# Kernel tuning notes

Measured on AMD Instinct MI355X. Metric: run time of the kernel, lower is better.

## Reference

```python
import jax, jax.numpy as jnp
import numpy as np

INPUT_SIZE = 512
HIDDEN_SIZE = 1024
UPDATE_BIAS = 1.0


def setup_inputs() -> dict:
    key = jax.random.key(0)
    k1, k2, k3, k4, k5 = jax.random.split(key, 5)
    B, T, I, H = 64, 512, INPUT_SIZE, HIDDEN_SIZE
    xh = I + H
    s = 1.0 / np.sqrt(xh)  # nn.Linear default init scale
    inp = {
        "input": jax.random.normal(k1, (B, T, I), dtype=jnp.float32),
        "h0": jnp.zeros((B, H), dtype=jnp.float32),
        "W_rz": jax.random.uniform(k2, (2 * H, xh), minval=-s, maxval=s, dtype=jnp.float32),
        "b_rz": jax.random.uniform(k3, (2 * H,), minval=-s, maxval=s, dtype=jnp.float32),
        "W_h": jax.random.uniform(k4, (H, xh), minval=-s, maxval=s, dtype=jnp.float32),
        "b_h": jax.random.uniform(k5, (H,), minval=-s, maxval=s, dtype=jnp.float32),
    }
    return inp


def _gru_scan(input, h0, W_rz, b_rz, W_h, b_h):
    H = h0.shape[-1]

    def step(h, x_t):
        # x_t: [B, I], h: [B, H]
        xh = jnp.concatenate([x_t, h], axis=1)          # [B, I+H]
        rz = xh @ W_rz.T + b_rz                          # [B, 2H]
        r = jax.nn.sigmoid(rz[:, :H])
        z = jax.nn.sigmoid(rz[:, H:] + UPDATE_BIAS)
        xrh = jnp.concatenate([x_t, r * h], axis=1)      # [B, I+H]
        hhat = jnp.tanh(xrh @ W_h.T + b_h)               # [B, H]
        h_new = z * h + (1.0 - z) * hhat
        return h_new, h_new

    xs = jnp.swapaxes(input, 0, 1)                       # [T, B, I]
    _, ys = jax.lax.scan(step, h0, xs)                   # ys: [T, B, H]
    return jnp.swapaxes(ys, 0, 1)                        # [B, T, H]


def reference(input, h0, W_rz, b_rz, W_h, b_h):
    return _gru_scan(input, h0, W_rz, b_rz, W_h, b_h)
```

## Files before the change

kernel.cpp:

```cpp
#include <hip/hip_runtime.h>
#include <hip/hip_bf16.h>

typedef __attribute__((ext_vector_type(8))) _Float16 f16x8;
typedef __attribute__((ext_vector_type(4))) float floatx4;

#define T_SEQ 512
#define B_SZ  64
#define I_SZ  512
#define H_SZ  1024
#define NC    3072
#define NGRP  4
#define WPG   64
#define POISON_U 0x7E007E00u
#define MF(a,b,c) __builtin_amdgcn_mfma_f32_16x16x32_f16((a),(b),(c),0,0,0)

static const size_t XPROJ_BYTES = (size_t)B_SZ * T_SEQ * NC * 2;
static const size_t EXC_OFF = XPROJ_BYTES;

__device__ __forceinline__ f16x8 cvt8(float4 a, float4 b) {
  f16x8 v;
  v[0] = (_Float16)a.x; v[1] = (_Float16)a.y; v[2] = (_Float16)a.z; v[3] = (_Float16)a.w;
  v[4] = (_Float16)b.x; v[5] = (_Float16)b.y; v[6] = (_Float16)b.z; v[7] = (_Float16)b.w;
  return v;
}

__device__ __forceinline__ f16x8 poison8() {
  union { unsigned u[4]; f16x8 v; } p;
  p.u[0] = p.u[1] = p.u[2] = p.u[3] = POISON_U;
  return p.v;
}

__global__ void init_kernel(const float* __restrict__ h0, unsigned* __restrict__ exc) {
  int i = blockIdx.x * blockDim.x + threadIdx.x;
  if (i >= NGRP * 32768) return;
  int grp = i >> 15;
  int wd  = i & 32767;
  int buf = wd >> 13;
  int wb  = wd & 8191;
  if (buf == 1) {
    int hf = wb * 2;
    int ct = hf >> 8, rem = hf & 255;
    int b = rem >> 4, kin = rem & 15;
    int k = ct * 16 + kin;
    int batch = grp * 16 + b;
    _Float16 lo = (_Float16)h0[(size_t)batch * H_SZ + k];
    _Float16 hi = (_Float16)h0[(size_t)batch * H_SZ + k + 1];
    exc[i] = (unsigned)__builtin_bit_cast(unsigned short, lo) |
             ((unsigned)__builtin_bit_cast(unsigned short, hi) << 16);
  } else {
    exc[i] = POISON_U;
  }
}

__global__ __launch_bounds__(256) void pregemm_kernel(
    const float* __restrict__ X, const float* __restrict__ Wrz,
    const float* __restrict__ Wh, const float* __restrict__ brz,
    const float* __restrict__ bh, _Float16* __restrict__ xproj) {
  __shared__ __align__(16) char smem[128 * 64 * 2];
  char* Asb = smem;
  char* Bsb = smem + 128 * 64;
  const int tid = threadIdx.x;
  const int w = tid >> 6, l = tid & 63;
  const int lg = l >> 4, ln = l & 15;
  const int wm = w >> 1, wn = w & 1;
  const int m0 = blockIdx.x * 128;
  const int n0 = blockIdx.y * 128;
  const int rs = tid >> 1;
  const int ks = (tid & 1) * 16;

  floatx4 acc[4][4];
#pragma unroll
  for (int i = 0; i < 4; i++)
#pragma unroll
    for (int j = 0; j < 4; j++) acc[i][j] = (floatx4){0.f, 0.f, 0.f, 0.f};

  const float* garow = X + (size_t)(m0 + rs) * I_SZ + ks;
  const int nrow = n0 + rs;
  const float* gbrow = (nrow < 2048) ? (Wrz + (size_t)nrow * 1536 + ks)
                                     : (Wh + (size_t)(nrow - 2048) * 1536 + ks);
  for (int kt = 0; kt < I_SZ; kt += 32) {
    float4 a0 = ((const float4*)(garow + kt))[0];
    float4 a1 = ((const float4*)(garow + kt))[1];
    float4 a2 = ((const float4*)(garow + kt))[2];
    float4 a3 = ((const float4*)(garow + kt))[3];
    float4 b0 = ((const float4*)(gbrow + kt))[0];
    float4 b1 = ((const float4*)(gbrow + kt))[1];
    float4 b2 = ((const float4*)(gbrow + kt))[2];
    float4 b3 = ((const float4*)(gbrow + kt))[3];
    __syncthreads();
    {
      int c0 = ks >> 3;
      f16x8* wp = (f16x8*)(Asb + rs * 64);
      wp[(c0)     ^ (rs & 3)] = cvt8(a0, a1);
      wp[(c0 + 1) ^ (rs & 3)] = cvt8(a2, a3);
      f16x8* wq = (f16x8*)(Bsb + rs * 64);
      wq[(c0)     ^ (rs & 3)] = cvt8(b0, b1);
      wq[(c0 + 1) ^ (rs & 3)] = cvt8(b2, b3);
    }
    __syncthreads();
    f16x8 af[4], bf[4];
#pragma unroll
    for (int i = 0; i < 4; i++) {
      int ra = wm * 64 + i * 16 + ln;
      af[i] = ((const f16x8*)(Asb + ra * 64))[lg ^ (ra & 3)];
      int rb = wn * 64 + i * 16 + ln;
      bf[i] = ((const f16x8*)(Bsb + rb * 64))[lg ^ (rb & 3)];
    }
#pragma unroll
    for (int i = 0; i < 4; i++)
#pragma unroll
      for (int j = 0; j < 4; j++)
        acc[i][j] = MF(af[i], bf[j], acc[i][j]);
  }
#pragma unroll
  for (int j = 0; j < 4; j++) {
    int n = n0 + wn * 64 + j * 16 + ln;
    float bias = (n < 2048) ? (brz[n] + ((n >= 1024) ? 1.0f : 0.0f)) : bh[n - 2048];
#pragma unroll
    for (int i = 0; i < 4; i++) {
      int mrow = m0 + wm * 64 + i * 16 + 4 * lg;
#pragma unroll
      for (int q = 0; q < 4; q++) {
        xproj[(size_t)(mrow + q) * NC + n] = (_Float16)(acc[i][j][q] + bias);
      }
    }
  }
}

#define ALD8C(X, P0, P1) do { asm volatile( \
  "global_load_dwordx4 %0, %8, off sc0 sc1\n\t" \
  "global_load_dwordx4 %1, %8, off offset:1024 sc0 sc1\n\t" \
  "global_load_dwordx4 %2, %8, off offset:2048 sc0 sc1\n\t" \
  "global_load_dwordx4 %3, %8, off offset:3072 sc0 sc1\n\t" \
  "global_load_dwordx4 %4, %9, off sc0 sc1\n\t" \
  "global_load_dwordx4 %5, %9, off offset:1024 sc0 sc1\n\t" \
  "global_load_dwordx4 %6, %9, off offset:2048 sc0 sc1\n\t" \
  "global_load_dwordx4 %7, %9, off offset:3072 sc0 sc1\n\t" \
  "s_waitcnt vmcnt(0)" \
  : "=&v"(X[0]), "=&v"(X[1]), "=&v"(X[2]), "=&v"(X[3]), \
    "=&v"(X[4]), "=&v"(X[5]), "=&v"(X[6]), "=&v"(X[7]) \
  : "v"(P0), "v"(P1) : "memory"); \
  __builtin_amdgcn_sched_barrier(0); } while (0)

#define VLD8C(X, P0, P1) do { \
  for (;;) { \
    ALD8C(X, P0, P1); \
    unsigned bad_ = 0; \
    _Pragma("unroll") for (int i_ = 0; i_ < 8; ++i_) { \
      union { f16x8 v; unsigned u[4]; } x_; x_.v = X[i_]; \
      _Pragma("unroll") for (int k_ = 0; k_ < 4; ++k_) \
        bad_ |= (x_.u[k_] == POISON_U); \
    } \
    if (__all((int)(bad_ == 0))) break; \
  } } while (0)

#define AST16(P, V) asm volatile( \
  "global_store_dwordx4 %0, %1, off sc0 sc1" :: "v"(P), "v"(V) : "memory")

__global__ __launch_bounds__(256) void gru_persistent_kernel(
    const float* __restrict__ Wrz, const float* __restrict__ Wh,
    const float* __restrict__ h0, const _Float16* __restrict__ xproj,
    float* __restrict__ Y, char* __restrict__ exc) {
  __shared__ __align__(16) char smem[48 * 2048 + 12288 + 512];
  floatx4* redR = (floatx4*)(smem + 98304);
  floatx4* redZ = redR + 256;
  floatx4* redB = redZ + 256;
  unsigned short* sm16 = (unsigned short*)(smem + 110592);

  const int bid = blockIdx.x;
  const int grp = bid >> 6;
  const int c   = bid & 63;
  const int tid = threadIdx.x;
  const int w = tid >> 6, l = tid & 63;
  const int lg = l >> 4, ln = l & 15;
  const int sw = ln & 7;
  const int colbase = 16 * c;
  const int jg = colbase + ln;
  const int b0 = 16 * grp;

  for (int it = tid; it < 48 * 128; it += 256) {
    int r = it >> 7, cc = it & 127;
    const float* src;
    if (r < 16)      src = Wrz + (size_t)(colbase + r) * 1536 + 512 + cc * 8;
    else if (r < 32) src = Wrz + (size_t)(1024 + colbase + (r - 16)) * 1536 + 512 + cc * 8;
    else             src = Wh  + (size_t)(colbase + (r - 32)) * 1536 + 512 + cc * 8;
    float4 f0 = ((const float4*)src)[0];
    float4 f1 = ((const float4*)src)[1];
    ((f16x8*)(smem + (size_t)r * 2048))[cc ^ (r & 7)] = cvt8(f0, f1);
  }
  __syncthreads();

  const f16x8* bpr = (const f16x8*)(smem + (size_t)ln * 2048);
  const f16x8* bpz = (const f16x8*)(smem + (size_t)(16 + ln) * 2048);
  const f16x8* bph = (const f16x8*)(smem + (size_t)(32 + ln) * 2048);

  char* gb = exc + (size_t)grp * 131072;

  const size_t rbase = (size_t)w * 8192 + (lg >> 1) * 512 + ln * 32 + (lg & 1) * 16;
  const size_t wbase = (size_t)c * 512 + l * 16;

  const f16x8 pz = poison8();

  float hm[4], zq[4], xr[4], xz[4], xh[4];
#define XPRE(T) { \
  _Pragma("unroll") for (int q_ = 0; q_ < 4; ++q_) { \
    size_t row_ = ((size_t)(b0 + 4 * lg + q_) * T_SEQ + (T)) * NC; \
    xr[q_] = (float)xproj[row_ + jg]; \
    xz[q_] = (float)xproj[row_ + 1024 + jg]; \
    xh[q_] = (float)xproj[row_ + 2048 + jg]; } }
  if (w == 0) {
#pragma unroll
    for (int q = 0; q < 4; ++q)
      hm[q] = h0[(size_t)(b0 + 4 * lg + q) * H_SZ + jg];
    XPRE(0)
  }

  for (int t = 0; t < T_SEQ; ++t) {
    const size_t wpo = (size_t)(t & 1) * 32768;
    const size_t rpo = 32768 - wpo;
    {
      f16x8 Af[8];
      VLD8C(Af, gb + rpo + rbase, gb + rpo + rbase + 4096);
      floatx4 ar = {0.f,0.f,0.f,0.f}, az = {0.f,0.f,0.f,0.f};
#pragma unroll
      for (int i = 0; i < 8; ++i) {
        int ki = 8 * w + i;
        ar = MF(Af[i], bpr[(4 * ki + lg) ^ sw], ar);
        az = MF(Af[i], bpz[(4 * ki + lg) ^ sw], az);
      }
      redR[tid] = ar;
      redZ[tid] = az;
    }
    __syncthreads();
    if (w == 0) {
      if (l < 32) AST16(gb + wpo + wbase, pz);
      floatx4 Dr = redR[l] + redR[64 + l] + redR[128 + l] + redR[192 + l];
      floatx4 Dz = redZ[l] + redZ[64 + l] + redZ[128 + l] + redZ[192 + l];
#pragma unroll
      for (int q = 0; q < 4; ++q) {
        float rr = 1.f / (1.f + __expf(-(Dr[q] + xr[q])));
        zq[q]    = 1.f / (1.f + __expf(-(Dz[q] + xz[q])));
        _Float16 hh = (_Float16)(rr * hm[q]);
        sm16[(4 * lg + q) * 16 + ln] = __builtin_bit_cast(unsigned short, hh);
      }
      asm volatile("s_waitcnt lgkmcnt(0)" ::: "memory");
      __builtin_amdgcn_sched_barrier(0);
      if (l < 32) {
        f16x8 v = *(const f16x8*)(sm16 + l * 8);
        asm volatile("s_waitcnt vmcnt(0)" ::: "memory");
        AST16(gb + 65536 + wpo + wbase, v);
      }
    }
    {
      f16x8 Bf[8];
      VLD8C(Bf, gb + 65536 + wpo + rbase, gb + 65536 + wpo + rbase + 4096);
      floatx4 ah = {0.f,0.f,0.f,0.f};
#pragma unroll
      for (int i = 0; i < 8; ++i) {
        int ki = 8 * w + i;
        ah = MF(Bf[i], bph[(4 * ki + lg) ^ sw], ah);
      }
      redB[tid] = ah;
    }
    __syncthreads();
    if (w == 0) {
      if (l < 32) AST16(gb + 65536 + rpo + wbase, pz);
      floatx4 Dh = redB[l] + redB[64 + l] + redB[128 + l] + redB[192 + l];
      float hnv[4];
#pragma unroll
      for (int q = 0; q < 4; ++q) {
        float hh = tanhf(Dh[q] + xh[q]);
        float hn = zq[q] * hm[q] + (1.f - zq[q]) * hh;
        hm[q] = hn; hnv[q] = hn;
        _Float16 hp = (_Float16)hn;
        sm16[(4 * lg + q) * 16 + ln] = __builtin_bit_cast(unsigned short, hp);
      }
      asm volatile("s_waitcnt lgkmcnt(0)" ::: "memory");
      __builtin_amdgcn_sched_barrier(0);
      if (l < 32) {
        f16x8 v = *(const f16x8*)(sm16 + l * 8);
        asm volatile("s_waitcnt vmcnt(0)" ::: "memory");
        AST16(gb + wpo + wbase, v);
      }
#pragma unroll
      for (int q = 0; q < 4; ++q)
        Y[((size_t)(b0 + 4 * lg + q) * T_SEQ + t) * H_SZ + jg] = hnv[q];
      if (t + 1 < T_SEQ) XPRE(t + 1)
    }
  }
}

extern "C" void kernel_launch(void* const* d_in, const int* in_sizes, int n_in,
                              void* d_out, int out_size, void* d_ws, size_t ws_size,
                              hipStream_t stream) {
  const float* X   = (const float*)d_in[0];
  const float* h0  = (const float*)d_in[1];
  const float* Wrz = (const float*)d_in[2];
  const float* brz = (const float*)d_in[3];
  const float* Wh  = (const float*)d_in[4];
  const float* bh  = (const float*)d_in[5];
  float* Y = (float*)d_out;
  char* ws = (char*)d_ws;

  _Float16* xproj = (_Float16*)(ws);
  char*     exc   = ws + EXC_OFF;

  hipLaunchKernelGGL(init_kernel, dim3(512), dim3(256), 0, stream,
                     h0, (unsigned*)exc);
  hipLaunchKernelGGL(pregemm_kernel, dim3(256, 24), dim3(256), 0, stream,
                     X, Wrz, Wh, brz, bh, xproj);

  void* kargs[] = { (void*)&Wrz, (void*)&Wh, (void*)&h0, (void*)&xproj,
                    (void*)&Y, (void*)&exc };
  hipError_t ce = hipLaunchCooperativeKernel((void*)gru_persistent_kernel,
                                             dim3(NGRP * WPG), dim3(256), kargs, 0, stream);
  if (ce != hipSuccess) {
    hipLaunchKernelGGL(gru_persistent_kernel, dim3(NGRP * WPG), dim3(256), 0, stream,
                       Wrz, Wh, h0, xproj, Y, exc);
  }
}
```

Baseline: 3.104 ms.

## Spread gate epilogue across all four waves instead of wave zero

The per-step gate math (reduction of partial MFMA sums, sigmoid, tanh, state update, exchange stores and output writes) previously ran only in wave 0 with four batch rows per lane. Each of the four waves now handles one row per lane, so the serial epilogue on the recurrent critical path is split four ways. Poison stores are moved to the other parity buffer, and the vmcnt wait before each exchange store is dropped. This changes the ordering assumptions of the cross-block flag/poison protocol, which risks races if the store ordering was relied on.

```diff
diff --git a/kernel.cpp b/kernel.cpp
--- a/kernel.cpp
+++ b/kernel.cpp
@@ -197,23 +197,24 @@
   char* gb = exc + (size_t)grp * 131072;
 
   const size_t rbase = (size_t)w * 8192 + (lg >> 1) * 512 + ln * 32 + (lg & 1) * 16;
-  const size_t wbase = (size_t)c * 512 + l * 16;
+  const size_t wslice = (size_t)c * 512 + w * 128 + (size_t)l * 16;
 
   const f16x8 pz = poison8();
 
-  float hm[4], zq[4], xr[4], xz[4], xh[4];
+  const int myb = b0 + 4 * w + lg;
+  const int rix = (w * 16 + ln) * 4 + lg;
+  float hm, zpre, xr, xz, xh;
 #define XPRE(T) { \
-  _Pragma("unroll") for (int q_ = 0; q_ < 4; ++q_) { \
-    size_t row_ = ((size_t)(b0 + 4 * lg + q_) * T_SEQ + (T)) * NC; \
-    xr[q_] = (float)xproj[row_ + jg]; \
-    xz[q_] = (float)xproj[row_ + 1024 + jg]; \
-    xh[q_] = (float)xproj[row_ + 2048 + jg]; } }
-  if (w == 0) {
-#pragma unroll
-    for (int q = 0; q < 4; ++q)
-      hm[q] = h0[(size_t)(b0 + 4 * lg + q) * H_SZ + jg];
-    XPRE(0)
-  }
+    size_t row_ = ((size_t)myb * T_SEQ + (T)) * NC; \
+    xr = (float)xproj[row_ + jg]; \
+    xz = (float)xproj[row_ + 1024 + jg]; \
+    xh = (float)xproj[row_ + 2048 + jg]; }
+  hm = h0[(size_t)myb * H_SZ + jg];
+  XPRE(0)
+
+  const float* rfR = (const float*)redR;
+  const float* rfZ = (const float*)redZ;
+  const float* rfB = (const float*)redB;
 
   for (int t = 0; t < T_SEQ; ++t) {
     const size_t wpo = (size_t)(t & 1) * 32768;
@@ -232,23 +233,19 @@
       redZ[tid] = az;
     }
     __syncthreads();
-    if (w == 0) {
-      if (l < 32) AST16(gb + wpo + wbase, pz);
-      floatx4 Dr = redR[l] + redR[64 + l] + redR[128 + l] + redR[192 + l];
-      floatx4 Dz = redZ[l] + redZ[64 + l] + redZ[128 + l] + redZ[192 + l];
-#pragma unroll
-      for (int q = 0; q < 4; ++q) {
-        float rr = 1.f / (1.f + __expf(-(Dr[q] + xr[q])));
-        zq[q]    = 1.f / (1.f + __expf(-(Dz[q] + xz[q])));
-        _Float16 hh = (_Float16)(rr * hm[q]);
-        sm16[(4 * lg + q) * 16 + ln] = __builtin_bit_cast(unsigned short, hh);
-      }
+    {
+      if (l < 8) AST16(gb + 65536 + rpo + wslice, pz);
+      float Dr = rfR[rix] + rfR[256 + rix] + rfR[512 + rix] + rfR[768 + rix];
+      float Dz = rfZ[rix] + rfZ[256 + rix] + rfZ[512 + rix] + rfZ[768 + rix];
+      float rr = 1.f / (1.f + __expf(-(Dr + xr)));
+      zpre = Dz + xz;
+      _Float16 hh = (_Float16)(rr * hm);
+      sm16[(4 * w + lg) * 16 + ln] = __builtin_bit_cast(unsigned short, hh);
       asm volatile("s_waitcnt lgkmcnt(0)" ::: "memory");
       __builtin_amdgcn_sched_barrier(0);
-      if (l < 32) {
-        f16x8 v = *(const f16x8*)(sm16 + l * 8);
-        asm volatile("s_waitcnt vmcnt(0)" ::: "memory");
-        AST16(gb + 65536 + wpo + wbase, v);
+      if (l < 8) {
+        f16x8 v = *(const f16x8*)(sm16 + w * 64 + l * 8);
+        AST16(gb + 65536 + wpo + wslice, v);
       }
     }
     {
@@ -263,28 +260,22 @@
       redB[tid] = ah;
     }
     __syncthreads();
-    if (w == 0) {
-      if (l < 32) AST16(gb + 65536 + rpo + wbase, pz);
-      floatx4 Dh = redB[l] + redB[64 + l] + redB[128 + l] + redB[192 + l];
-      float hnv[4];
-#pragma unroll
-      for (int q = 0; q < 4; ++q) {
-        float hh = tanhf(Dh[q] + xh[q]);
-        float hn = zq[q] * hm[q] + (1.f - zq[q]) * hh;
-        hm[q] = hn; hnv[q] = hn;
-        _Float16 hp = (_Float16)hn;
-        sm16[(4 * lg + q) * 16 + ln] = __builtin_bit_cast(unsigned short, hp);
-      }
+    {
+      if (l < 8) AST16(gb + rpo + wslice, pz);
+      float Dh = rfB[rix] + rfB[256 + rix] + rfB[512 + rix] + rfB[768 + rix];
+      float z  = 1.f / (1.f + __expf(-zpre));
+      float hhat = tanhf(Dh + xh);
+      float hn = z * hm + (1.f - z) * hhat;
+      hm = hn;
+      _Float16 hp = (_Float16)hn;
+      sm16[(4 * w + lg) * 16 + ln] = __builtin_bit_cast(unsigned short, hp);
       asm volatile("s_waitcnt lgkmcnt(0)" ::: "memory");
       __builtin_amdgcn_sched_barrier(0);
-      if (l < 32) {
-        f16x8 v = *(const f16x8*)(sm16 + l * 8);
-        asm volatile("s_waitcnt vmcnt(0)" ::: "memory");
-        AST16(gb + wpo + wbase, v);
-      }
-#pragma unroll
-      for (int q = 0; q < 4; ++q)
-        Y[((size_t)(b0 + 4 * lg + q) * T_SEQ + t) * H_SZ + jg] = hnv[q];
+      if (l < 8) {
+        f16x8 v = *(const f16x8*)(sm16 + w * 64 + l * 8);
+        AST16(gb + wpo + wslice, v);
+      }
+      Y[((size_t)myb * T_SEQ + t) * H_SZ + jg] = hn;
       if (t + 1 < T_SEQ) XPRE(t + 1)
     }
   }
```

After: 3.094 ms. About the same (-0.3%).
